# Optimization experiments

Hardware: AMD Instinct MI355X
Metric: run time of the kernel (lower is better)

The kernel has to match this reference:

```python
import jax, jax.numpy as jnp
import numpy as np

I = 256   # input_size
H = 256   # hidden_size
B = 64
T = 2048


def setup_inputs() -> dict:
    key = jax.random.key(0)
    ks = jax.random.split(key, 7)
    s_i = 1.0 / np.sqrt(I)
    s_h = 1.0 / np.sqrt(H)
    return {
        "x": jax.random.normal(ks[0], (B, T, I), dtype=jnp.float32),
        "h0": jax.random.normal(ks[1], (1, B, H), dtype=jnp.float32),
        "c0": jax.random.normal(ks[2], (1, B, H), dtype=jnp.float32),
        # Only l_fi / l_fh affect the output in the original forward (all four
        # gates are computed from the same pre-activation due to a source bug).
        "W_fi": jax.random.uniform(ks[3], (H, I), jnp.float32, -s_i, s_i),
        "b_fi": jax.random.uniform(ks[4], (H,), jnp.float32, -s_i, s_i),
        "W_fh": jax.random.uniform(ks[5], (H, H), jnp.float32, -s_h, s_h),
        "b_fh": jax.random.uniform(ks[6], (H,), jnp.float32, -s_h, s_h),
    }


def reference(x, h0, c0, W_fi, b_fi, W_fh, b_fh):
    # Faithful to the buggy torch source:
    #   f = i = o = sigmoid(l_fi(x_t) + l_fh(ht_1)); m = tanh(same)
    #   ht_1, ct_1 are NEVER updated -> no recurrence; vectorize over time.
    ht_1 = h0[0]  # (B, H), state[0].squeeze(0)
    ct_1 = c0[0]  # (B, H)
    gx = jnp.einsum('bti,hi->bth', x, W_fi) + b_fi          # (B, T, H)
    gh = ht_1 @ W_fh.T + b_fh                               # (B, H)
    g = gx + gh[:, None, :]                                 # (B, T, H)
    s = jax.nn.sigmoid(g)
    m = jnp.tanh(g)
    c = s * ct_1[:, None, :] + s * m                        # c_t per step
    h = s * jnp.tanh(c)                                     # h_t per step
    hidden_seq = jnp.transpose(h, (1, 0, 2))                # (T, B, H), cat dim=0
    return (hidden_seq, (h[:, -1, :], c[:, -1, :]))
```

## Files before the change

kernel.cpp:

```cpp
#include <hip/hip_runtime.h>
#include <hip/hip_bf16.h>
#include <stdint.h>

#define T_SZ 2048
#define B_SZ 64
#define H_SZ 256
#define I_SZ 256
#define M_SZ (B_SZ * T_SZ)
#define TBH  (T_SZ * B_SZ * H_SZ)

typedef float f32x4 __attribute__((ext_vector_type(4)));
typedef short s16x8 __attribute__((ext_vector_type(8)));

__device__ __forceinline__ unsigned pack_bf16(float a, float b) {
    unsigned ua = __float_as_uint(a);
    unsigned ub = __float_as_uint(b);
    ua += 0x7fffu + ((ua >> 16) & 1u);
    ub += 0x7fffu + ((ub >> 16) & 1u);
    return (ua >> 16) | (ub & 0xffff0000u);
}

__device__ __forceinline__ void gload_lds16(const unsigned short* g, unsigned short* l) {
    __builtin_amdgcn_global_load_lds(
        (const __attribute__((address_space(1))) unsigned int*)g,
        (__attribute__((address_space(3))) unsigned int*)l,
        16, 0, 0);
}

__global__ void prep_kernel(const float* __restrict__ h0,
                            const float* __restrict__ W_fi,
                            const float* __restrict__ b_fi,
                            const float* __restrict__ W_fh,
                            const float* __restrict__ b_fh,
                            unsigned short* __restrict__ Wb,
                            float* __restrict__ gb) {
    __shared__ float h0s[H_SZ];
    const int b = blockIdx.x;
    const int h = threadIdx.x;
    h0s[h] = h0[b * H_SZ + h];
    __syncthreads();
    const float4* w4 = (const float4*)(W_fh + (size_t)h * H_SZ);
    float acc = 0.f;
#pragma unroll 8
    for (int j = 0; j < H_SZ / 4; ++j) {
        float4 w = w4[j];
        acc = fmaf(w.x, h0s[4 * j + 0], acc);
        acc = fmaf(w.y, h0s[4 * j + 1], acc);
        acc = fmaf(w.z, h0s[4 * j + 2], acc);
        acc = fmaf(w.w, h0s[4 * j + 3], acc);
    }
    gb[b * H_SZ + h] = acc + b_fi[h] + b_fh[h];

    const int e = (b * 256 + h) * 4;
    float4 wv = *(const float4*)(W_fi + e);
    uint2 pk;
    pk.x = pack_bf16(wv.x, wv.y);
    pk.y = pack_bf16(wv.z, wv.w);
    *(uint2*)(Wb + e) = pk;
}

__global__ __launch_bounds__(256) void lstm_main(
    const float* __restrict__ x,
    const unsigned short* __restrict__ Wb,
    const float* __restrict__ gb,
    const float* __restrict__ c0,
    float* __restrict__ out) {
    __shared__ __align__(16) unsigned short As[128 * 32];
    __shared__ __align__(16) unsigned short Bs[128 * 32];

    const int tid  = threadIdx.x;
    const int lane = tid & 63;
    const int wid  = tid >> 6;
    const int bid  = blockIdx.x;
    const int mt = bid >> 1, nt = bid & 1;
    const int m0 = mt * 128, n0 = nt * 128;
    const int wm = (wid & 1) * 64, wn = (wid >> 1) * 64;

    f32x4 acc[4][4];
#pragma unroll
    for (int mi = 0; mi < 4; ++mi)
#pragma unroll
        for (int ni = 0; ni < 4; ++ni)
            acc[mi][ni] = (f32x4){0.f, 0.f, 0.f, 0.f};

    const int am = tid >> 2, aq = tid & 3;
    const float* aptr0 = x + (size_t)(m0 + am) * I_SZ + aq * 8;
    const float* aptr1 = aptr0 + (size_t)64 * I_SZ;

    const int bslot0 = wid * 64 + lane;
    const int bslot1 = 256 + bslot0;
    const int br0 = bslot0 >> 2, bq0 = bslot0 & 3;
    const int br1 = bslot1 >> 2, bq1 = bslot1 & 3;
    const unsigned short* bsrc0 = Wb + (size_t)(n0 + br0) * I_SZ + bq0 * 8;
    const unsigned short* bsrc1 = Wb + (size_t)(n0 + br1) * I_SZ + bq1 * 8;
    unsigned short* bdst0 = Bs + (size_t)(wid * 64) * 8;
    unsigned short* bdst1 = Bs + (size_t)(256 + wid * 64) * 8;

    const int fr = lane & 15;
    const int fq = lane >> 4;

    for (int kt = 0; kt < 8; ++kt) {
        const int kof = kt * 32;
        if (kt) __syncthreads();

        const float4* p0 = (const float4*)(aptr0 + kof);
        const float4* p1 = (const float4*)(aptr1 + kof);
        float4 v0 = p0[0], v1 = p0[1];
        float4 v2 = p1[0], v3 = p1[1];

        gload_lds16(bsrc0 + kof, bdst0);
        gload_lds16(bsrc1 + kof, bdst1);

        uint4 pa, pb;
        pa.x = pack_bf16(v0.x, v0.y); pa.y = pack_bf16(v0.z, v0.w);
        pa.z = pack_bf16(v1.x, v1.y); pa.w = pack_bf16(v1.z, v1.w);
        pb.x = pack_bf16(v2.x, v2.y); pb.y = pack_bf16(v2.z, v2.w);
        pb.z = pack_bf16(v3.x, v3.y); pb.w = pack_bf16(v3.z, v3.w);
        *(uint4*)(As + (size_t)tid * 8) = pa;
        *(uint4*)(As + (size_t)(256 + tid) * 8) = pb;

        __syncthreads();

        s16x8 af[4], bf[4];
#pragma unroll
        for (int mi = 0; mi < 4; ++mi)
            af[mi] = *(const s16x8*)(As + (wm + mi * 16 + fr) * 32 + fq * 8);
#pragma unroll
        for (int ni = 0; ni < 4; ++ni)
            bf[ni] = *(const s16x8*)(Bs + (wn + ni * 16 + fr) * 32 + fq * 8);
#pragma unroll
        for (int mi = 0; mi < 4; ++mi)
#pragma unroll
            for (int ni = 0; ni < 4; ++ni)
                acc[mi][ni] = __builtin_amdgcn_mfma_f32_16x16x32_bf16(
                    af[mi], bf[ni], acc[mi][ni], 0, 0, 0);
    }

    const int coln = n0 + wn + fr;
#pragma unroll
    for (int mi = 0; mi < 4; ++mi) {
#pragma unroll
        for (int r = 0; r < 4; ++r) {
            const int Mg = m0 + wm + mi * 16 + fq * 4 + r;
            const int bb = Mg >> 11;
            const int tt = Mg & (T_SZ - 1);
            const int obase = tt * (B_SZ * H_SZ) + bb * H_SZ;
            const float* gbrow = gb + bb * H_SZ;
            const float* c0row = c0 + bb * H_SZ;
            const bool last = (tt == T_SZ - 1);
#pragma unroll
            for (int ni = 0; ni < 4; ++ni) {
                const int h = coln + ni * 16;
                float g = acc[mi][ni][r] + gbrow[h];
                float gc = fminf(15.f, fmaxf(-15.f, g));
                float e = __expf(-gc);
                float s = __builtin_amdgcn_rcpf(1.f + e);
                float e2 = e * e;
                float m = (1.f - e2) * __builtin_amdgcn_rcpf(1.f + e2);
                float cv = s * (c0row[h] + m);
                float cc = fminf(15.f, fmaxf(-15.f, cv));
                float ec = __expf(-2.f * cc);
                float th = (1.f - ec) * __builtin_amdgcn_rcpf(1.f + ec);
                float hv = s * th;
                out[obase + h] = hv;
                if (last) {
                    out[TBH + bb * H_SZ + h] = hv;
                    out[TBH + B_SZ * H_SZ + bb * H_SZ + h] = cv;
                }
            }
        }
    }
}

extern "C" void kernel_launch(void* const* d_in, const int* in_sizes, int n_in,
                              void* d_out, int out_size, void* d_ws, size_t ws_size,
                              hipStream_t stream) {
    const float* x    = (const float*)d_in[0];
    const float* h0   = (const float*)d_in[1];
    const float* c0   = (const float*)d_in[2];
    const float* W_fi = (const float*)d_in[3];
    const float* b_fi = (const float*)d_in[4];
    const float* W_fh = (const float*)d_in[5];
    const float* b_fh = (const float*)d_in[6];
    float* out = (float*)d_out;

    unsigned short* Wb = (unsigned short*)d_ws;
    float* gb = (float*)((char*)d_ws + 131072);

    hipLaunchKernelGGL(prep_kernel, dim3(B_SZ), dim3(H_SZ), 0, stream,
                       h0, W_fi, b_fi, W_fh, b_fh, Wb, gb);
    hipLaunchKernelGGL(lstm_main, dim3(M_SZ / 128 * 2), dim3(256), 0, stream,
                       x, Wb, gb, c0, out);
}
```

Baseline: 276.7 us.

## Load MFMA operands directly from global into registers, drop LDS staging

```diff
diff --git a/kernel.cpp b/kernel.cpp
--- a/kernel.cpp
+++ b/kernel.cpp
@@ -18,13 +18,6 @@
     ua += 0x7fffu + ((ua >> 16) & 1u);
     ub += 0x7fffu + ((ub >> 16) & 1u);
     return (ua >> 16) | (ub & 0xffff0000u);
-}
-
-__device__ __forceinline__ void gload_lds16(const unsigned short* g, unsigned short* l) {
-    __builtin_amdgcn_global_load_lds(
-        (const __attribute__((address_space(1))) unsigned int*)g,
-        (__attribute__((address_space(3))) unsigned int*)l,
-        16, 0, 0);
 }
 
 __global__ void prep_kernel(const float* __restrict__ h0,
@@ -59,22 +52,26 @@
     *(uint2*)(Wb + e) = pk;
 }
 
-__global__ __launch_bounds__(256) void lstm_main(
+__global__ __launch_bounds__(256, 3) void lstm_main(
     const float* __restrict__ x,
     const unsigned short* __restrict__ Wb,
     const float* __restrict__ gb,
     const float* __restrict__ c0,
     float* __restrict__ out) {
-    __shared__ __align__(16) unsigned short As[128 * 32];
-    __shared__ __align__(16) unsigned short Bs[128 * 32];
-
     const int tid  = threadIdx.x;
     const int lane = tid & 63;
     const int wid  = tid >> 6;
-    const int bid  = blockIdx.x;
-    const int mt = bid >> 1, nt = bid & 1;
+
+    const int orig = blockIdx.x;
+    const int mt = (orig >> 4) * 8 + (orig & 7);
+    const int nt = (orig >> 3) & 1;
     const int m0 = mt * 128, n0 = nt * 128;
     const int wm = (wid & 1) * 64, wn = (wid >> 1) * 64;
+    const int fr = lane & 15;
+    const int fq = lane >> 4;
+
+    const float* abase = x + (size_t)(m0 + wm + fr) * I_SZ + fq * 8;
+    const unsigned short* bbase = Wb + (size_t)(n0 + wn + fr) * I_SZ + fq * 8;
 
     f32x4 acc[4][4];
 #pragma unroll
@@ -83,51 +80,42 @@
         for (int ni = 0; ni < 4; ++ni)
             acc[mi][ni] = (f32x4){0.f, 0.f, 0.f, 0.f};
 
-    const int am = tid >> 2, aq = tid & 3;
-    const float* aptr0 = x + (size_t)(m0 + am) * I_SZ + aq * 8;
-    const float* aptr1 = aptr0 + (size_t)64 * I_SZ;
+    float4 alo[4], ahi[4];
+#pragma unroll
+    for (int mi = 0; mi < 4; ++mi) {
+        const float4* p = (const float4*)(abase + mi * 16 * I_SZ);
+        alo[mi] = p[0];
+        ahi[mi] = p[1];
+    }
 
-    const int bslot0 = wid * 64 + lane;
-    const int bslot1 = 256 + bslot0;
-    const int br0 = bslot0 >> 2, bq0 = bslot0 & 3;
-    const int br1 = bslot1 >> 2, bq1 = bslot1 & 3;
-    const unsigned short* bsrc0 = Wb + (size_t)(n0 + br0) * I_SZ + bq0 * 8;
-    const unsigned short* bsrc1 = Wb + (size_t)(n0 + br1) * I_SZ + bq1 * 8;
-    unsigned short* bdst0 = Bs + (size_t)(wid * 64) * 8;
-    unsigned short* bdst1 = Bs + (size_t)(256 + wid * 64) * 8;
-
-    const int fr = lane & 15;
-    const int fq = lane >> 4;
-
+#pragma unroll
     for (int kt = 0; kt < 8; ++kt) {
-        const int kof = kt * 32;
-        if (kt) __syncthreads();
-
-        const float4* p0 = (const float4*)(aptr0 + kof);
-        const float4* p1 = (const float4*)(aptr1 + kof);
-        float4 v0 = p0[0], v1 = p0[1];
-        float4 v2 = p1[0], v3 = p1[1];
-
-        gload_lds16(bsrc0 + kof, bdst0);
-        gload_lds16(bsrc1 + kof, bdst1);
-
-        uint4 pa, pb;
-        pa.x = pack_bf16(v0.x, v0.y); pa.y = pack_bf16(v0.z, v0.w);
-        pa.z = pack_bf16(v1.x, v1.y); pa.w = pack_bf16(v1.z, v1.w);
-        pb.x = pack_bf16(v2.x, v2.y); pb.y = pack_bf16(v2.z, v2.w);
-        pb.z = pack_bf16(v3.x, v3.y); pb.w = pack_bf16(v3.z, v3.w);
-        *(uint4*)(As + (size_t)tid * 8) = pa;
-        *(uint4*)(As + (size_t)(256 + tid) * 8) = pb;
-
-        __syncthreads();
-
-        s16x8 af[4], bf[4];
-#pragma unroll
-        for (int mi = 0; mi < 4; ++mi)
-            af[mi] = *(const s16x8*)(As + (wm + mi * 16 + fr) * 32 + fq * 8);
+        s16x8 bf[4];
 #pragma unroll
         for (int ni = 0; ni < 4; ++ni)
-            bf[ni] = *(const s16x8*)(Bs + (wn + ni * 16 + fr) * 32 + fq * 8);
+            bf[ni] = *(const s16x8*)(bbase + ni * 16 * I_SZ + kt * 32);
+
+        s16x8 af[4];
+#pragma unroll
+        for (int mi = 0; mi < 4; ++mi) {
+            union { s16x8 v; __hip_bfloat162 h[4]; } u;
+            u.h[0] = __float22bfloat162_rn(make_float2(alo[mi].x, alo[mi].y));
+            u.h[1] = __float22bfloat162_rn(make_float2(alo[mi].z, alo[mi].w));
+            u.h[2] = __float22bfloat162_rn(make_float2(ahi[mi].x, ahi[mi].y));
+            u.h[3] = __float22bfloat162_rn(make_float2(ahi[mi].z, ahi[mi].w));
+            af[mi] = u.v;
+        }
+
+        if (kt < 7) {
+            const int kof = (kt + 1) * 32;
+#pragma unroll
+            for (int mi = 0; mi < 4; ++mi) {
+                const float4* p = (const float4*)(abase + mi * 16 * I_SZ + kof);
+                alo[mi] = p[0];
+                ahi[mi] = p[1];
+            }
+        }
+
 #pragma unroll
         for (int mi = 0; mi < 4; ++mi)
 #pragma unroll
@@ -137,27 +125,31 @@
     }
 
     const int coln = n0 + wn + fr;
+    const int bb = (m0 + wm) >> 11;
+    float gbv[4], c0v[4];
+#pragma unroll
+    for (int ni = 0; ni < 4; ++ni) {
+        gbv[ni] = gb[bb * H_SZ + coln + ni * 16];
+        c0v[ni] = c0[bb * H_SZ + coln + ni * 16];
+    }
 #pragma unroll
     for (int mi = 0; mi < 4; ++mi) {
 #pragma unroll
         for (int r = 0; r < 4; ++r) {
             const int Mg = m0 + wm + mi * 16 + fq * 4 + r;
-            const int bb = Mg >> 11;
             const int tt = Mg & (T_SZ - 1);
             const int obase = tt * (B_SZ * H_SZ) + bb * H_SZ;
-            const float* gbrow = gb + bb * H_SZ;
-            const float* c0row = c0 + bb * H_SZ;
             const bool last = (tt == T_SZ - 1);
 #pragma unroll
             for (int ni = 0; ni < 4; ++ni) {
                 const int h = coln + ni * 16;
-                float g = acc[mi][ni][r] + gbrow[h];
+                float g = acc[mi][ni][r] + gbv[ni];
                 float gc = fminf(15.f, fmaxf(-15.f, g));
                 float e = __expf(-gc);
                 float s = __builtin_amdgcn_rcpf(1.f + e);
                 float e2 = e * e;
                 float m = (1.f - e2) * __builtin_amdgcn_rcpf(1.f + e2);
-                float cv = s * (c0row[h] + m);
+                float cv = s * (c0v[ni] + m);
                 float cc = fminf(15.f, fmaxf(-15.f, cv));
                 float ec = __expf(-2.f * cc);
                 float th = (1.f - ec) * __builtin_amdgcn_rcpf(1.f + ec);
```

Result: slower. 318.0 us (+14.9%).
